# Performance work log

Measured on AMD Instinct MI355X. Metric: run time of the kernel, lower is better.

The kernel has to match this reference:

```python
import jax, jax.numpy as jnp
import numpy as np

NUM_NUM = 32    # numerical (pass-through) features
NUM_CAT = 32    # embedded categorical features
CARD = 128      # one-hot width per categorical feature
OUT = 32        # per-feature embedding output dim (0.25 * 128)
BATCH = 16384


def setup_inputs() -> dict:
    key = jax.random.key(0)
    k1, k2, k3 = jax.random.split(key, 3)
    x = jax.random.normal(k1, (BATCH, NUM_NUM + NUM_CAT * CARD), dtype=jnp.float32)
    # stacked per-feature nn.Linear(CARD, OUT) weights/biases (all same shape)
    W = jax.random.normal(k2, (NUM_CAT, CARD, OUT), dtype=jnp.float32) / np.sqrt(CARD).astype(np.float32)
    b = jax.random.normal(k3, (NUM_CAT, OUT), dtype=jnp.float32) * 0.01
    return {"x": x, "W": W, "b": b}


def reference(x, W, b):
    # Numerical columns pass through unchanged; each categorical one-hot slice
    # goes through its own small Linear, then everything is concatenated.
    # Since all categorical slices have identical width, the per-feature loop of
    # small GEMMs is expressed as one batched (block-diagonal) matmul.
    x_num = x[..., :NUM_NUM]                                      # [B, 32]
    x_cat = x[..., NUM_NUM:].reshape(x.shape[:-1] + (NUM_CAT, CARD))  # [B, F, C]
    emb = jnp.einsum('bfc,fco->bfo', x_cat, W) + b                # [B, F, OUT]
    emb = emb.reshape(x.shape[:-1] + (NUM_CAT * OUT,))            # [B, 1024]
    return jnp.concatenate([x_num, emb], axis=-1)                 # [B, 1056]
```

## Files before the change

### kernel.cpp

```cpp
#include <hip/hip_runtime.h>

#define BATCH   16384
#define NUM_NUM 32
#define NUM_CAT 32
#define CARD    128
#define OUT_F   32
#define XSTRIDE (NUM_NUM + NUM_CAT * CARD)
#define OSTRIDE (NUM_NUM + NUM_CAT * OUT_F)

#define TR   256
#define CK   32
#define XPAD (CK + 1)

__global__ __launch_bounds__(256, 1) void emb_gemm(const float* __restrict__ x,
                                                   const float* __restrict__ W,
                                                   const float* __restrict__ bias,
                                                   float* __restrict__ out) {
    __shared__ float w_s[CARD][OUT_F];
    __shared__ float x_s[TR][XPAD];

    const int f    = blockIdx.y;
    const int row0 = blockIdx.x * TR;
    const int tid  = threadIdx.x;

    {
        const float4* wg  = (const float4*)(W + (size_t)f * CARD * OUT_F);
        float4*       ws4 = (float4*)&w_s[0][0];
#pragma unroll
        for (int i = 0; i < 4; ++i) ws4[i * 256 + tid] = wg[i * 256 + tid];
    }

    const int og = tid & 7;
    const int rg = tid >> 3;

    float acc[8][4];
#pragma unroll
    for (int j = 0; j < 8; ++j)
#pragma unroll
        for (int k = 0; k < 4; ++k) acc[j][k] = 0.0f;

    const float* xg_base = x + (size_t)row0 * XSTRIDE + NUM_NUM + f * CARD;

    for (int ck = 0; ck < CARD / CK; ++ck) {
        const float* xg = xg_base + ck * CK;
#pragma unroll
        for (int it = 0; it < 8; ++it) {
            int    idx = it * 256 + tid;
            int    r   = idx >> 3;
            int    c4  = (idx & 7) * 4;
            float4 v   = *(const float4*)(xg + (size_t)r * XSTRIDE + c4);
            x_s[r][c4 + 0] = v.x;
            x_s[r][c4 + 1] = v.y;
            x_s[r][c4 + 2] = v.z;
            x_s[r][c4 + 3] = v.w;
        }
        __syncthreads();

#pragma unroll 8
        for (int c = 0; c < CK; ++c) {
            float4 w4 = *(const float4*)&w_s[ck * CK + c][og * 4];
#pragma unroll
            for (int j = 0; j < 8; ++j) {
                float xv = x_s[rg * 8 + j][c];
                acc[j][0] += xv * w4.x;
                acc[j][1] += xv * w4.y;
                acc[j][2] += xv * w4.z;
                acc[j][3] += xv * w4.w;
            }
        }
        __syncthreads();
    }

    float4 b4 = *(const float4*)(bias + f * OUT_F + og * 4);
#pragma unroll
    for (int j = 0; j < 8; ++j) {
        int    row = row0 + rg * 8 + j;
        float4 o4;
        o4.x = acc[j][0] + b4.x;
        o4.y = acc[j][1] + b4.y;
        o4.z = acc[j][2] + b4.z;
        o4.w = acc[j][3] + b4.w;
        *(float4*)(out + (size_t)row * OSTRIDE + NUM_NUM + f * OUT_F + og * 4) = o4;
    }
}

__global__ __launch_bounds__(256) void num_copy(const float* __restrict__ x,
                                                float* __restrict__ out) {
    int    idx = blockIdx.x * 256 + threadIdx.x;
    int    row = idx >> 3;
    int    c4  = (idx & 7) * 4;
    float4 v   = *(const float4*)(x + (size_t)row * XSTRIDE + c4);
    *(float4*)(out + (size_t)row * OSTRIDE + c4) = v;
}

extern "C" void kernel_launch(void* const* d_in, const int* in_sizes, int n_in,
                              void* d_out, int out_size, void* d_ws, size_t ws_size,
                              hipStream_t stream) {
    const float* x    = (const float*)d_in[0];
    const float* W    = (const float*)d_in[1];
    const float* bias = (const float*)d_in[2];
    float*       out  = (float*)d_out;

    dim3 grid(BATCH / TR, NUM_CAT);
    emb_gemm<<<grid, 256, 0, stream>>>(x, W, bias, out);
    num_copy<<<BATCH * 8 / 256, 256, 0, stream>>>(x, out);
}
```

Before: 95.89 us.

## Register-prefetch x tiles, enlarge row tile, 8x8 microtile, fuse numeric copy

The GEMM kernel now prefetches the next x chunk into registers while computing the current one, which overlaps global loads with FMA work. Each block covers 512 rows with 16-column chunks, and each thread computes an 8x8 output tile from float4 shared-memory reads. Launch bounds now allow 2 blocks per CU. The separate numeric pass-through kernel is folded into the f==0 blocks to save a launch. The costs are higher register pressure and a larger shared footprint, and a padding of 20 may cause some bank conflicts.

Measured after the change: 174.3 us. +81.8%, slower.

```diff
diff --git a/kernel.cpp b/kernel.cpp
--- a/kernel.cpp
+++ b/kernel.cpp
@@ -8,20 +8,24 @@
 #define XSTRIDE (NUM_NUM + NUM_CAT * CARD)
 #define OSTRIDE (NUM_NUM + NUM_CAT * OUT_F)
 
-#define TR   256
-#define CK   32
-#define XPAD (CK + 1)
+#define TRB   512
+#define CK    16
+#define XPAD  20
+#define NCHUNK (CARD / CK)
 
-__global__ __launch_bounds__(256, 1) void emb_gemm(const float* __restrict__ x,
+__global__ __launch_bounds__(256, 2) void emb_gemm(const float* __restrict__ x,
                                                    const float* __restrict__ W,
                                                    const float* __restrict__ bias,
                                                    float* __restrict__ out) {
     __shared__ float w_s[CARD][OUT_F];
-    __shared__ float x_s[TR][XPAD];
+    __shared__ float x_s[TRB][XPAD];
 
     const int f    = blockIdx.y;
-    const int row0 = blockIdx.x * TR;
+    const int row0 = blockIdx.x * TRB;
     const int tid  = threadIdx.x;
+
+    const int og = tid & 3;
+    const int rg = tid >> 2;
 
     {
         const float4* wg  = (const float4*)(W + (size_t)f * CARD * OUT_F);
@@ -30,67 +34,101 @@
         for (int i = 0; i < 4; ++i) ws4[i * 256 + tid] = wg[i * 256 + tid];
     }
 
-    const int og = tid & 7;
-    const int rg = tid >> 3;
+    const float* xg_base = x + (size_t)row0 * XSTRIDE + NUM_NUM + f * CARD;
 
-    float acc[8][4];
+    float4 st[8];
+#pragma unroll
+    for (int it = 0; it < 8; ++it) {
+        int idx = it * 256 + tid;
+        int r   = idx >> 2;
+        int c4  = (idx & 3) << 2;
+        st[it]  = *(const float4*)(xg_base + (size_t)r * XSTRIDE + c4);
+    }
+#pragma unroll
+    for (int it = 0; it < 8; ++it) {
+        int idx = it * 256 + tid;
+        *(float4*)&x_s[idx >> 2][(idx & 3) << 2] = st[it];
+    }
+    __syncthreads();
+
+    float acc[8][8];
 #pragma unroll
     for (int j = 0; j < 8; ++j)
 #pragma unroll
-        for (int k = 0; k < 4; ++k) acc[j][k] = 0.0f;
+        for (int k = 0; k < 8; ++k) acc[j][k] = 0.0f;
 
-    const float* xg_base = x + (size_t)row0 * XSTRIDE + NUM_NUM + f * CARD;
-
-    for (int ck = 0; ck < CARD / CK; ++ck) {
-        const float* xg = xg_base + ck * CK;
+    for (int ck = 0; ck < NCHUNK; ++ck) {
+        if (ck < NCHUNK - 1) {
+            const float* xg = xg_base + (ck + 1) * CK;
 #pragma unroll
-        for (int it = 0; it < 8; ++it) {
-            int    idx = it * 256 + tid;
-            int    r   = idx >> 3;
-            int    c4  = (idx & 7) * 4;
-            float4 v   = *(const float4*)(xg + (size_t)r * XSTRIDE + c4);
-            x_s[r][c4 + 0] = v.x;
-            x_s[r][c4 + 1] = v.y;
-            x_s[r][c4 + 2] = v.z;
-            x_s[r][c4 + 3] = v.w;
-        }
-        __syncthreads();
-
-#pragma unroll 8
-        for (int c = 0; c < CK; ++c) {
-            float4 w4 = *(const float4*)&w_s[ck * CK + c][og * 4];
-#pragma unroll
-            for (int j = 0; j < 8; ++j) {
-                float xv = x_s[rg * 8 + j][c];
-                acc[j][0] += xv * w4.x;
-                acc[j][1] += xv * w4.y;
-                acc[j][2] += xv * w4.z;
-                acc[j][3] += xv * w4.w;
+            for (int it = 0; it < 8; ++it) {
+                int idx = it * 256 + tid;
+                int r   = idx >> 2;
+                int c4  = (idx & 3) << 2;
+                st[it]  = *(const float4*)(xg + (size_t)r * XSTRIDE + c4);
             }
         }
+
+#pragma unroll 2
+        for (int cs = 0; cs < CK; cs += 4) {
+            float4 xv[8];
+#pragma unroll
+            for (int j = 0; j < 8; ++j) xv[j] = *(const float4*)&x_s[rg * 8 + j][cs];
+#pragma unroll
+            for (int cc = 0; cc < 4; ++cc) {
+                const int c  = ck * CK + cs + cc;
+                float4 w0 = *(const float4*)&w_s[c][og * 8];
+                float4 w1 = *(const float4*)&w_s[c][og * 8 + 4];
+#pragma unroll
+                for (int j = 0; j < 8; ++j) {
+                    float xf = ((const float*)&xv[j])[cc];
+                    acc[j][0] += xf * w0.x;
+                    acc[j][1] += xf * w0.y;
+                    acc[j][2] += xf * w0.z;
+                    acc[j][3] += xf * w0.w;
+                    acc[j][4] += xf * w1.x;
+                    acc[j][5] += xf * w1.y;
+                    acc[j][6] += xf * w1.z;
+                    acc[j][7] += xf * w1.w;
+                }
+            }
+        }
+
         __syncthreads();
+        if (ck < NCHUNK - 1) {
+#pragma unroll
+            for (int it = 0; it < 8; ++it) {
+                int idx = it * 256 + tid;
+                *(float4*)&x_s[idx >> 2][(idx & 3) << 2] = st[it];
+            }
+            __syncthreads();
+        }
     }
 
-    float4 b4 = *(const float4*)(bias + f * OUT_F + og * 4);
+    float4 b0 = *(const float4*)(bias + f * OUT_F + og * 8);
+    float4 b1 = *(const float4*)(bias + f * OUT_F + og * 8 + 4);
 #pragma unroll
     for (int j = 0; j < 8; ++j) {
-        int    row = row0 + rg * 8 + j;
-        float4 o4;
-        o4.x = acc[j][0] + b4.x;
-        o4.y = acc[j][1] + b4.y;
-        o4.z = acc[j][2] + b4.z;
-        o4.w = acc[j][3] + b4.w;
-        *(float4*)(out + (size_t)row * OSTRIDE + NUM_NUM + f * OUT_F + og * 4) = o4;
+        size_t obase = (size_t)(row0 + rg * 8 + j) * OSTRIDE + NUM_NUM + f * OUT_F + og * 8;
+        float4 o0, o1;
+        o0.x = acc[j][0] + b0.x; o0.y = acc[j][1] + b0.y;
+        o0.z = acc[j][2] + b0.z; o0.w = acc[j][3] + b0.w;
+        o1.x = acc[j][4] + b1.x; o1.y = acc[j][5] + b1.y;
+        o1.z = acc[j][6] + b1.z; o1.w = acc[j][7] + b1.w;
+        *(float4*)(out + obase)     = o0;
+        *(float4*)(out + obase + 4) = o1;
     }
-}
 
-__global__ __launch_bounds__(256) void num_copy(const float* __restrict__ x,
-                                                float* __restrict__ out) {
-    int    idx = blockIdx.x * 256 + threadIdx.x;
-    int    row = idx >> 3;
-    int    c4  = (idx & 7) * 4;
-    float4 v   = *(const float4*)(x + (size_t)row * XSTRIDE + c4);
-    *(float4*)(out + (size_t)row * OSTRIDE + c4) = v;
+    if (f == 0) {
+#pragma unroll
+        for (int it = 0; it < 16; ++it) {
+            int idx = it * 256 + tid;
+            int r   = idx >> 3;
+            int c4  = (idx & 7) << 2;
+            *(float4*)(out + (size_t)(row0 + r) * OSTRIDE + c4) =
+                *(const float4*)(x + (size_t)(row0 + r) * XSTRIDE + c4);
+        }
+    }
 }
 
 extern "C" void kernel_launch(void* const* d_in, const int* in_sizes, int n_in,
@@ -101,7 +139,6 @@
     const float* bias = (const float*)d_in[2];
     float*       out  = (float*)d_out;
 
-    dim3 grid(BATCH / TR, NUM_CAT);
+    dim3 grid(BATCH / TRB, NUM_CAT);
     emb_gemm<<<grid, 256, 0, stream>>>(x, W, bias, out);
-    num_copy<<<BATCH * 8 / 256, 256, 0, stream>>>(x, out);
 }
```
